# Optimization experiments

Measured on AMD Instinct MI355X. Metric: run time of the kernel, lower is better.

The kernel has to match this reference:

```python
import jax, jax.numpy as jnp
import numpy as np

D = 256       # vec_dim
HEADS = 8     # head_num
PS = 4        # patch_size
WS = 7        # window_size (in patches)
P = WS * WS   # tokens per window


def _relative_index():
    # replicates the torch meshgrid / relative coord logic (indexing='ij')
    coords = np.stack(np.meshgrid(np.arange(WS), np.arange(WS), indexing='ij'))  # [2,WS,WS]
    cf = coords.reshape(2, -1)                                                   # [2,P]
    rc = (cf[:, :, None] - cf[:, None, :]).transpose(1, 2, 0)                    # [P,P,2]
    rc[:, :, 0] += WS - 1
    rc[:, :, 1] += WS - 1
    rc[:, :, 1] *= 2 * WS - 1
    return rc.sum(-1)  # [P,P] ints in [0,(2WS-1)^2)


def _shift_mask(ch, cw):
    # standard swin shift mask built on the patch grid (ch, cw)
    fm = np.zeros((ch, cw))
    idx = (slice(0, -WS), slice(-WS, -(WS // 2)), slice(-(WS // 2), None))
    cnt = 0
    for y in idx:
        for x in idx:
            fm[y, x] = cnt
            cnt += 1
    nh, nw = ch // WS, cw // WS
    fm = fm.reshape(nh, WS, nw, WS).transpose(0, 2, 1, 3).reshape(nh * nw, P)
    m = fm[:, None, :] - fm[:, :, None]
    return np.where(m != 0, -100.0, 0.0).astype(np.float32)


def setup_inputs() -> dict:
    key = jax.random.key(0)
    ks = jax.random.split(key, 10)
    N, PN = 8, 3136
    s = 0.02
    return {
        'inputs': jax.random.normal(ks[0], (N, D, PN), jnp.float32),
        'Wk': jax.random.normal(ks[1], (HEADS * D, D), jnp.float32) * s,
        'bk': jax.random.normal(ks[2], (HEADS * D,), jnp.float32) * s,
        'Wq': jax.random.normal(ks[3], (HEADS * D, D), jnp.float32) * s,
        'bq': jax.random.normal(ks[4], (HEADS * D,), jnp.float32) * s,
        'Wv': jax.random.normal(ks[5], (HEADS * D, D), jnp.float32) * s,
        'bv': jax.random.normal(ks[6], (HEADS * D,), jnp.float32) * s,
        'Wo': jax.random.normal(ks[7], (D, HEADS * D), jnp.float32) * s,
        'bo': jax.random.normal(ks[8], (D,), jnp.float32) * s,
        'rel_code': jax.random.normal(ks[9], ((2 * WS - 1) ** 2, HEADS), jnp.float32) * 0.02,
        'h': 224,
        'w': 224,
    }


def _forward(inputs, Wk, bk, Wq, bq, Wv, bv, Wo, bo, rel_code, h, w):
    ch, cw = h // PS, w // PS            # patch grid
    N, _, PN = inputs.shape
    C = D // (PS * PS)
    nh, nw = ch // WS, cw // WS
    WIN = nh * nw

    # patches2features -> pixel-space roll by WS//2 -> features2patches
    x = inputs.reshape(N, C, PS, PS, ch, cw)
    x = x.transpose(0, 1, 4, 2, 5, 3).reshape(N, C, ch * PS, cw * PS)
    x = jnp.roll(x, (WS // 2, WS // 2), axis=(-2, -1))
    x = x.reshape(N, C, ch, PS, cw, PS).transpose(0, 2, 4, 1, 3, 5).reshape(N, PN, D)
    x = x.transpose(0, 2, 1)  # [N,D,PN]

    def proj(W, b):
        e = jnp.einsum('od,ndp->nop', W, x) + b[None, :, None]  # [N,HEADS*D,PN]
        e = e.reshape(N, HEADS, D, ch, cw)
        # window partition: n h d (nh w1)(nw w2) -> n h (nh nw) d (w1 w2)
        e = e.reshape(N, HEADS, D, nh, WS, nw, WS)
        return e.transpose(0, 1, 3, 5, 2, 4, 6).reshape(N, HEADS, WIN, D, P)

    k = proj(Wk, bk)
    q = proj(Wq, bq)
    v = proj(Wv, bv)

    # attn[p,q] = k_p . q_q  (softmax over keys p, axis=3)
    attn = jnp.einsum('nhgdp,nhgdq->nhgpq', k, q) / (D ** 0.5)
    mask = jnp.asarray(_shift_mask(ch, cw))
    attn = attn + mask[None, None]
    rel_idx = _relative_index().ravel()
    rel = rel_code[rel_idx].reshape(P, P, HEADS).transpose(2, 0, 1)  # [H,P,P]
    attn = attn + rel[None, :, None]
    wmap = jax.nn.softmax(attn, axis=3)

    out = jnp.einsum('nhgdp,nhgpq->nhgdq', v, wmap)
    # window merge back to [N,H,D,PN]
    out = out.reshape(N, HEADS, nh, nw, D, WS, WS)
    out = out.transpose(0, 1, 4, 2, 5, 3, 6).reshape(N, HEADS * D, PN)
    return jnp.einsum('od,ndp->nop', Wo, out) + bo[None, :, None]  # [N,D,PN]


def reference(inputs, Wk, bk, Wq, bq, Wv, bv, Wo, bo, rel_code, h, w):
    return _forward(inputs, Wk, bk, Wq, bq, Wv, bv, Wo, bo, rel_code, h, w)
```

## Files before the change

### kernel.cpp

```cpp
#include <hip/hip_runtime.h>
#include <hip/hip_bf16.h>


#define NBATCH 8
#define MSTR   2176
#define TROWS  3200

typedef unsigned short ushort_t;
typedef __attribute__((ext_vector_type(8))) short bf16x8;
typedef __attribute__((ext_vector_type(8))) unsigned short u16x8;
typedef __attribute__((ext_vector_type(4))) float f32x4;

__device__ __forceinline__ float b2f(ushort_t u) {
  union { unsigned int i; float f; } v; v.i = ((unsigned int)u) << 16; return v.f;
}
__device__ __forceinline__ ushort_t f2b(float f) {
  union { float f; unsigned int u; } v; v.f = f;
  unsigned int u = v.u;
  return (ushort_t)((u + 0x7FFFu + ((u >> 16) & 1u)) >> 16);
}
__device__ __forceinline__ int regof(int y) { return (y < 49) ? 0 : ((y < 53) ? 1 : 2); }
__device__ __forceinline__ int div7(int t) { return (t * 37) >> 8; }
__device__ __forceinline__ int tmap(int p, int gi, int gj) {
  int wi = div7(p); return (gi * 7 + wi) * 56 + gj * 7 + (p - wi * 7);
}
__device__ __forceinline__ ushort4 pack4(f32x4 a) {
  ushort4 u; u.x = f2b(a[0]); u.y = f2b(a[1]); u.z = f2b(a[2]); u.w = f2b(a[3]);
  return u;
}

__global__ void k_prep(const float* __restrict__ Wk, const float* __restrict__ Wq,
                       const float* __restrict__ Wo, const float* __restrict__ Wv,
                       const float* __restrict__ bk, const float* __restrict__ bq,
                       const float* __restrict__ bv, const float* __restrict__ bo,
                       const float* __restrict__ relc,
                       ushort_t* __restrict__ Aext, ushort_t* __restrict__ Wov3,
                       float* __restrict__ cvec, float* __restrict__ relL2) {
  __shared__ float red[8];
  int blk = blockIdx.x, t = threadIdx.x;
  if (blk < 512) {
    int h = blk >> 6, b0 = (blk & 63) << 2, a = t;
    const float* wkh = Wk + h * 65536;
    const float* wqh = Wq + h * 65536;
    float a0 = 0.f, a1 = 0.f, a2 = 0.f, a3 = 0.f;
    for (int dd = 0; dd < 256; ++dd) {
      float wk = wkh[dd * 256 + a];
      float4 w4 = *(const float4*)(wqh + dd * 256 + b0);
      a0 += wk * w4.x; a1 += wk * w4.y; a2 += wk * w4.z; a3 += wk * w4.w;
    }
    ushort4 u; u.x = f2b(a0); u.y = f2b(a1); u.z = f2b(a2); u.w = f2b(a3);
    *(ushort4*)(Aext + (h * 256 + a) * 256 + b0) = u;
  } else if (blk < 1024) {
    int bb = blk - 512;
    int h = bb >> 6, o0 = (bb & 63) << 2, d = t;
    float a0 = 0.f, a1 = 0.f, a2 = 0.f, a3 = 0.f;
    for (int dd = 0; dd < 256; ++dd) {
      float wv = Wv[(h * 256 + dd) * 256 + d];
      a0 += Wo[(o0 + 0) * 2048 + h * 256 + dd] * wv;
      a1 += Wo[(o0 + 1) * 2048 + h * 256 + dd] * wv;
      a2 += Wo[(o0 + 2) * 2048 + h * 256 + dd] * wv;
      a3 += Wo[(o0 + 3) * 2048 + h * 256 + dd] * wv;
    }
    Wov3[(o0 + 0) * 2048 + h * 256 + d] = f2b(a0);
    Wov3[(o0 + 1) * 2048 + h * 256 + d] = f2b(a1);
    Wov3[(o0 + 2) * 2048 + h * 256 + d] = f2b(a2);
    Wov3[(o0 + 3) * 2048 + h * 256 + d] = f2b(a3);
  } else if (blk < 1032) {
    int h = blk - 1024;
    float s1 = 0.f, s2 = 0.f;
    for (int dd = 0; dd < 256; ++dd) {
      s1 += bk[h * 256 + dd] * Wq[(h * 256 + dd) * 256 + t];
      s2 += bq[h * 256 + dd] * Wk[(h * 256 + dd) * 256 + t];
    }
    Aext[(2048 + h) * 256 + t] = f2b(s1);
    Aext[(2056 + h) * 256 + t] = f2b(s2);
  } else if (blk == 1032) {
    for (int i = t; i < 112 * 256 / 8; i += 256)
      *(u16x8*)(Aext + 2064 * 256 + i * 8) = (u16x8){0,0,0,0,0,0,0,0};
  } else if (blk < 1289) {
    int o = blk - 1033;
    const float* wob = Wo + o * 2048;
    float acc = 0.f;
#pragma unroll
    for (int j = 0; j < 8; ++j) acc += wob[j * 256 + t] * bv[j * 256 + t];
#pragma unroll
    for (int s = 1; s < 64; s <<= 1) acc += __shfl_xor(acc, s);
    if ((t & 63) == 0) red[t >> 6] = acc;
    __syncthreads();
    if (t == 0) cvec[o] = bo[o] + red[0] + red[1] + red[2] + red[3];
  } else {
    if (t < 8) {
      float c = 0.f;
      for (int dd = 0; dd < 256; ++dd) c += bk[t * 256 + dd] * bq[t * 256 + dd];
      red[t] = c * 0.0625f;
    }
    __syncthreads();
    for (int i = t; i < 8 * 169; i += 256) {
      int h = i / 169, idx = i - h * 169;
      relL2[i] = relc[idx * 8 + h] + red[h];
    }
  }
}

__global__ void k_conv(const float* __restrict__ X, ushort_t* __restrict__ Xroll) {
  const int n = blockIdx.x / 57, y = blockIdx.x % 57;
  const int tid = threadIdx.x;
  ushort_t* xr = Xroll + (size_t)n * TROWS * 256;
  if (y == 56) {
    for (int i = tid; i < 64 * 256 / 8; i += 256)
      *(u16x8*)(xr + 3136 * 256 + i * 8) = (u16x8){0,0,0,0,0,0,0,0};
    return;
  }
  const int wave = tid >> 6, x = tid & 63;
  const float* xin = X + (size_t)n * 256 * 3136;
  const int ty_m = (y == 0) ? 55 : y - 1;
  const int tx_m = (x == 0) ? 55 : x - 1;
  for (int dd = 0; dd < 64; ++dd) {
    int d = wave * 64 + dd;
    int c = d >> 4, p1 = (d >> 2) & 3, p2 = d & 3;
    int sp = c * 16 + (((p1 + 1) & 3) << 2) + ((p2 + 1) & 3);
    int ty = (p1 == 3) ? y : ty_m;
    int tx = (p2 == 3) ? x : tx_m;
    if (x < 56)
      xr[(y * 56 + x) * 256 + d] = f2b(xin[sp * 3136 + ty * 56 + tx]);
  }
}

__global__ __launch_bounds__(256, 2) void k_gemm1(
    const ushort_t* __restrict__ Xroll, const ushort_t* __restrict__ Aext,
    ushort_t* __restrict__ MT) {
  __shared__ ushort_t Asm[128 * 72];
  __shared__ ushort_t Bsm[128 * 72];
  const int bx = blockIdx.x;
  const int n = bx / 425, r = bx % 425;
  const int tt = r / 17, aa = r % 17;
  const int a0 = aa * 128, t0 = tt * 128;
  const int tid = threadIdx.x, wave = tid >> 6, lane = tid & 63;
  const int quad = lane >> 4, l16 = lane & 15;
  const int wa = wave >> 1, wt = wave & 1;
  const ushort_t* Xn = Xroll + (size_t)n * TROWS * 256;
  ushort_t* Mn = MT + (size_t)n * TROWS * MSTR;

  const int sr = tid >> 1, sc = (tid & 1) * 4;
  bf16x8 ra[4], rb[4];
#pragma unroll
  for (int i = 0; i < 4; ++i) {
    ra[i] = *(const bf16x8*)(Aext + (a0 + sr) * 256 + (sc + i) * 8);
    rb[i] = *(const bf16x8*)(Xn + (t0 + sr) * 256 + (sc + i) * 8);
  }

  f32x4 acc[4][4];
#pragma unroll
  for (int i = 0; i < 4; ++i)
#pragma unroll
    for (int j = 0; j < 4; ++j) acc[i][j] = (f32x4){0.f, 0.f, 0.f, 0.f};

  for (int kit = 0; kit < 4; ++kit) {
#pragma unroll
    for (int i = 0; i < 4; ++i) {
      *(bf16x8*)(&Asm[sr * 72 + (sc + i) * 8]) = ra[i];
      *(bf16x8*)(&Bsm[sr * 72 + (sc + i) * 8]) = rb[i];
    }
    __syncthreads();
    if (kit < 3) {
      int k0 = (kit + 1) * 64;
#pragma unroll
      for (int i = 0; i < 4; ++i) {
        ra[i] = *(const bf16x8*)(Aext + (a0 + sr) * 256 + k0 + (sc + i) * 8);
        rb[i] = *(const bf16x8*)(Xn + (t0 + sr) * 256 + k0 + (sc + i) * 8);
      }
    }
#pragma unroll
    for (int kk = 0; kk < 2; ++kk) {
      bf16x8 af[4], bf[4];
#pragma unroll
      for (int i = 0; i < 4; ++i)
        af[i] = *(const bf16x8*)(&Asm[(wa * 64 + i * 16 + l16) * 72 + kk * 32 + quad * 8]);
#pragma unroll
      for (int j = 0; j < 4; ++j)
        bf[j] = *(const bf16x8*)(&Bsm[(wt * 64 + j * 16 + l16) * 72 + kk * 32 + quad * 8]);
#pragma unroll
      for (int i = 0; i < 4; ++i)
#pragma unroll
        for (int j = 0; j < 4; ++j)
          acc[i][j] = __builtin_amdgcn_mfma_f32_16x16x32_bf16(af[i], bf[j], acc[i][j], 0, 0, 0);
    }
    __syncthreads();
  }
#pragma unroll
  for (int i = 0; i < 4; ++i)
#pragma unroll
    for (int j = 0; j < 4; ++j) {
      int tg = t0 + wt * 64 + j * 16 + l16;
      int ag = a0 + wa * 64 + i * 16 + quad * 4;
      *(ushort4*)(Mn + (size_t)tg * MSTR + ag) = pack4(acc[i][j]);
    }
}

#define XP_STR 264
__global__ __launch_bounds__(512, 4) void k_attn2(
    const ushort_t* __restrict__ Xroll, ushort_t* __restrict__ MT,
    const float* __restrict__ relL2) {
  __shared__ ushort_t Xp[64 * XP_STR];
  __shared__ ushort_t StB[2][64 * 72];
  __shared__ float aqsL[8 * 64];
  __shared__ float bpsL[8 * 64];
  __shared__ float relLh[8 * 169];

  const int tid = threadIdx.x;
  const int wave = tid >> 6, lane = tid & 63;
  const int quad = lane >> 4, l16 = lane & 15;
  const int group = wave >> 2, wv = wave & 3;
  const int n = blockIdx.x >> 6, g = blockIdx.x & 63;
  const int gi = g >> 3, gj = g & 7;
  const ushort_t* Xn = Xroll + (size_t)n * TROWS * 256;
  ushort_t* Mn = MT + (size_t)n * TROWS * MSTR;

  {
    const int p = tid & 63, cg = tid >> 6;
    if (p < 49) {
      int t = tmap(p, gi, gj);
#pragma unroll
      for (int i = 0; i < 4; ++i)
        *(u16x8*)(&Xp[p * XP_STR + (cg * 4 + i) * 8]) =
            *(const u16x8*)(Xn + t * 256 + (cg * 4 + i) * 8);
    } else {
#pragma unroll
      for (int i = 0; i < 4; ++i)
        *(u16x8*)(&Xp[p * XP_STR + (cg * 4 + i) * 8]) = (u16x8){0,0,0,0,0,0,0,0};
    }
  }
  for (int i = tid; i < 8 * 169; i += 512) relLh[i] = relL2[i];
  {
    const int h = tid >> 6, q = tid & 63;
    int qq = (q < 49) ? q : 48;
    int t = tmap(qq, gi, gj);
    aqsL[h * 64 + q] = b2f(Mn[(size_t)t * MSTR + 2048 + h]);
    bpsL[h * 64 + q] = b2f(Mn[(size_t)t * MSTR + 2056 + h]);
  }
  __syncthreads();

  bf16x8 xfr[4][2];
#pragma unroll
  for (int dt = 0; dt < 4; ++dt) {
    const int d = (wv * 4 + dt) * 16 + l16;
#pragma unroll
    for (int kk = 0; kk < 2; ++kk)
#pragma unroll
      for (int j = 0; j < 8; ++j)
        xfr[dt][kk][j] = (short)Xp[(kk * 32 + quad * 8 + j) * XP_STR + d];
  }

  const int q = wv * 16 + l16;
  const int qq = (q < 49) ? q : 48;
  const int tq = tmap(qq, gi, gj);
  const ushort_t* Mbase = Mn + (size_t)tq * MSTR + quad * 8;
  const int yq = div7(qq), xq = qq - yq * 7;
  const int fq = regof(gi * 7 + yq) * 3 + regof(gj * 7 + xq);

  for (int hh = 0; hh < 4; ++hh) {
    const int h = hh * 2 + group;
    f32x4 sacc[4];
#pragma unroll
    for (int pt = 0; pt < 4; ++pt) sacc[pt] = (f32x4){0.f, 0.f, 0.f, 0.f};
    const ushort_t* mrow = Mbase + h * 256;
#pragma unroll
    for (int kk = 0; kk < 8; ++kk) {
      bf16x8 bfm = *(const bf16x8*)(mrow + kk * 32);
#pragma unroll
      for (int pt = 0; pt < 4; ++pt) {
        bf16x8 af = *(const bf16x8*)(&Xp[(pt * 16 + l16) * XP_STR + kk * 32 + quad * 8]);
        sacc[pt] = __builtin_amdgcn_mfma_f32_16x16x32_bf16(af, bfm, sacc[pt], 0, 0, 0);
      }
    }
    float v[16];
    const float aqv = aqsL[h * 64 + q];
    const float* rel_h = &relLh[h * 169];
    float m = -1e30f;
#pragma unroll
    for (int pt = 0; pt < 4; ++pt)
#pragma unroll
      for (int r = 0; r < 4; ++r) {
        int p = pt * 16 + quad * 4 + r;
        float val = -1e30f;
        if (p < 49) {
          int yp = div7(p), xp = p - yp * 7;
          int fp = regof(gi * 7 + yp) * 3 + regof(gj * 7 + xp);
          val = (sacc[pt][r] + aqv + bpsL[h * 64 + p]) * 0.0625f +
                rel_h[(yp - yq + 6) + 13 * (xp - xq + 6)];
          if (fp != fq) val -= 100.f;
        }
        v[pt * 4 + r] = val;
        m = fmaxf(m, val);
      }
    m = fmaxf(m, __shfl_xor(m, 16));
    m = fmaxf(m, __shfl_xor(m, 32));
    float s = 0.f;
#pragma unroll
    for (int i = 0; i < 16; ++i) { v[i] = __expf(v[i] - m); s += v[i]; }
    s += __shfl_xor(s, 16);
    s += __shfl_xor(s, 32);
    const float inv = 1.f / s;
    __syncthreads();
    {
      ushort_t* sb = &StB[group][q * 72];
#pragma unroll
      for (int pt = 0; pt < 4; ++pt) {
        ushort4 u;
        u.x = f2b(v[pt * 4 + 0] * inv); u.y = f2b(v[pt * 4 + 1] * inv);
        u.z = f2b(v[pt * 4 + 2] * inv); u.w = f2b(v[pt * 4 + 3] * inv);
        *(ushort4*)(&sb[pt * 16 + quad * 4]) = u;
      }
    }
    __syncthreads();
#pragma unroll
    for (int qt = 0; qt < 4; ++qt) {
      f32x4 tacc[4];
#pragma unroll
      for (int dt = 0; dt < 4; ++dt) tacc[dt] = (f32x4){0.f, 0.f, 0.f, 0.f};
#pragma unroll
      for (int kk = 0; kk < 2; ++kk) {
        bf16x8 bfw = *(const bf16x8*)(&StB[group][(qt * 16 + l16) * 72 + kk * 32 + quad * 8]);
#pragma unroll
        for (int dt = 0; dt < 4; ++dt)
          tacc[dt] = __builtin_amdgcn_mfma_f32_16x16x32_bf16(xfr[dt][kk], bfw, tacc[dt], 0, 0, 0);
      }
      int q2 = qt * 16 + l16;
      if (q2 < 49) {
        int t2 = tmap(q2, gi, gj);
#pragma unroll
        for (int dt = 0; dt < 4; ++dt) {
          int d0 = (wv * 4 + dt) * 16 + quad * 4;
          *(ushort4*)(Mn + (size_t)t2 * MSTR + h * 256 + d0) = pack4(tacc[dt]);
        }
      }
    }
  }
}

__global__ __launch_bounds__(256, 4) void k_gemm3(
    const ushort_t* __restrict__ Wov3, const ushort_t* __restrict__ MT,
    const float* __restrict__ cvec, float* __restrict__ out) {
  __shared__ ushort_t Asm[128 * 72];
  __shared__ ushort_t Bsm[64 * 72];
  const int bx = blockIdx.x;
  const int n = bx / 98, r = bx % 98;
  const int oi = r / 49, tt = r % 49;
  const int o0 = oi * 128, t0 = tt * 64;
  const int tid = threadIdx.x, wave = tid >> 6, lane = tid & 63;
  const int quad = lane >> 4, l16 = lane & 15;
  const ushort_t* Tn = MT + (size_t)n * TROWS * MSTR;
  float* on = out + (size_t)n * 256 * 3136;

  const int arA = tid >> 1, acA = (tid & 1) * 4;
  const int arB = tid >> 2, acB = (tid & 3) * 2;
  bf16x8 ra[4], rb[2];
#pragma unroll
  for (int i = 0; i < 4; ++i)
    ra[i] = *(const bf16x8*)(Wov3 + (o0 + arA) * 2048 + (acA + i) * 8);
#pragma unroll
  for (int i = 0; i < 2; ++i)
    rb[i] = *(const bf16x8*)(Tn + (size_t)(t0 + arB) * MSTR + (acB + i) * 8);

  f32x4 acc[2][4];
#pragma unroll
  for (int i = 0; i < 2; ++i)
#pragma unroll
    for (int j = 0; j < 4; ++j) acc[i][j] = (f32x4){0.f, 0.f, 0.f, 0.f};

  for (int kit = 0; kit < 32; ++kit) {
#pragma unroll
    for (int i = 0; i < 4; ++i) *(bf16x8*)(&Asm[arA * 72 + (acA + i) * 8]) = ra[i];
#pragma unroll
    for (int i = 0; i < 2; ++i) *(bf16x8*)(&Bsm[arB * 72 + (acB + i) * 8]) = rb[i];
    __syncthreads();
    if (kit < 31) {
      int k0 = (kit + 1) * 64;
#pragma unroll
      for (int i = 0; i < 4; ++i)
        ra[i] = *(const bf16x8*)(Wov3 + (o0 + arA) * 2048 + k0 + (acA + i) * 8);
#pragma unroll
      for (int i = 0; i < 2; ++i)
        rb[i] = *(const bf16x8*)(Tn + (size_t)(t0 + arB) * MSTR + k0 + (acB + i) * 8);
    }
#pragma unroll
    for (int kk = 0; kk < 2; ++kk) {
      bf16x8 af[2], bf[4];
#pragma unroll
      for (int i = 0; i < 2; ++i)
        af[i] = *(const bf16x8*)(&Asm[((wave * 2 + i) * 16 + l16) * 72 + kk * 32 + quad * 8]);
#pragma unroll
      for (int j = 0; j < 4; ++j)
        bf[j] = *(const bf16x8*)(&Bsm[(j * 16 + l16) * 72 + kk * 32 + quad * 8]);
#pragma unroll
      for (int i = 0; i < 2; ++i)
#pragma unroll
        for (int j = 0; j < 4; ++j)
          acc[i][j] = __builtin_amdgcn_mfma_f32_16x16x32_bf16(af[i], bf[j], acc[i][j], 0, 0, 0);
    }
    __syncthreads();
  }
#pragma unroll
  for (int i = 0; i < 2; ++i) {
    const int ob = o0 + (wave * 2 + i) * 16 + quad * 4;
    const float4 cv = *(const float4*)(cvec + ob);
#pragma unroll
    for (int j = 0; j < 4; ++j) {
      const int tg = t0 + j * 16 + l16;
      on[(size_t)(ob + 0) * 3136 + tg] = acc[i][j][0] + cv.x;
      on[(size_t)(ob + 1) * 3136 + tg] = acc[i][j][1] + cv.y;
      on[(size_t)(ob + 2) * 3136 + tg] = acc[i][j][2] + cv.z;
      on[(size_t)(ob + 3) * 3136 + tg] = acc[i][j][3] + cv.w;
    }
  }
}

extern "C" void kernel_launch(void* const* d_in, const int* in_sizes, int n_in,
                              void* d_out, int out_size, void* d_ws, size_t ws_size,
                              hipStream_t stream) {
  (void)in_sizes; (void)n_in; (void)out_size; (void)ws_size;
  const float* X  = (const float*)d_in[0];
  const float* Wk = (const float*)d_in[1];
  const float* bk = (const float*)d_in[2];
  const float* Wq = (const float*)d_in[3];
  const float* bq = (const float*)d_in[4];
  const float* Wv = (const float*)d_in[5];
  const float* bv = (const float*)d_in[6];
  const float* Wo = (const float*)d_in[7];
  const float* bo = (const float*)d_in[8];
  const float* rc = (const float*)d_in[9];

  ushort_t* MT    = (ushort_t*)d_ws;
  ushort_t* Xroll = MT + (size_t)8 * TROWS * MSTR;
  ushort_t* Aext  = Xroll + (size_t)8 * TROWS * 256;
  ushort_t* Wov3  = Aext + 2176 * 256;
  float* fbase = (float*)(Wov3 + 256 * 2048);
  float* cvec  = fbase;
  float* relL2 = fbase + 256;
  float* out = (float*)d_out;

  k_prep <<<dim3(1290), dim3(256), 0, stream>>>(Wk, Wq, Wo, Wv, bk, bq, bv, bo, rc,
                                                Aext, Wov3, cvec, relL2);
  k_conv <<<dim3(8 * 57), dim3(256), 0, stream>>>(X, Xroll);
  k_gemm1<<<dim3(8 * 425), dim3(256), 0, stream>>>(Xroll, Aext, MT);
  k_attn2<<<dim3(8 * 64), dim3(512), 0, stream>>>(Xroll, MT, relL2);
  k_gemm3<<<dim3(8 * 98), dim3(256), 0, stream>>>(Wov3, MT, cvec, out);
}
```

Baseline: 341.1 us.

## Use direct global-to-LDS loads with XOR swizzle in GEMMs and rework conv gather

The two GEMM kernels now load tiles straight into LDS with global_load_lds and an XOR-swizzled layout instead of staging through registers into padded shared arrays. gemm1 loads the whole 128x256 X tile once and streams the A operand from global into registers with a one-step prefetch. gemm3 moves to 128x128 tiles with a K step of 128 and a bounds guard on tokens. The conv kernel changes from one thread per pixel to one thread per channel, walking x. This cuts register staging and sync overhead but drops the overlap between loading and compute in gemm3, and the bigger LDS footprint lowers occupancy.

After: 317.0 us. 1.08x faster.

```diff
diff --git a/kernel.cpp b/kernel.cpp
--- a/kernel.cpp
+++ b/kernel.cpp
@@ -27,6 +27,11 @@
 __device__ __forceinline__ ushort4 pack4(f32x4 a) {
   ushort4 u; u.x = f2b(a[0]); u.y = f2b(a[1]); u.z = f2b(a[2]); u.w = f2b(a[3]);
   return u;
+}
+__device__ __forceinline__ void gload_lds16(const ushort_t* g, ushort_t* l) {
+  __builtin_amdgcn_global_load_lds(
+      (const __attribute__((address_space(1))) void*)g,
+      (__attribute__((address_space(3))) void*)l, 16, 0, 0);
 }
 
 __global__ void k_prep(const float* __restrict__ Wk, const float* __restrict__ Wq,
@@ -104,33 +109,28 @@
 
 __global__ void k_conv(const float* __restrict__ X, ushort_t* __restrict__ Xroll) {
   const int n = blockIdx.x / 57, y = blockIdx.x % 57;
-  const int tid = threadIdx.x;
   ushort_t* xr = Xroll + (size_t)n * TROWS * 256;
+  const int d = threadIdx.x;
   if (y == 56) {
-    for (int i = tid; i < 64 * 256 / 8; i += 256)
+    for (int i = d; i < 64 * 256 / 8; i += 256)
       *(u16x8*)(xr + 3136 * 256 + i * 8) = (u16x8){0,0,0,0,0,0,0,0};
     return;
   }
-  const int wave = tid >> 6, x = tid & 63;
-  const float* xin = X + (size_t)n * 256 * 3136;
-  const int ty_m = (y == 0) ? 55 : y - 1;
-  const int tx_m = (x == 0) ? 55 : x - 1;
-  for (int dd = 0; dd < 64; ++dd) {
-    int d = wave * 64 + dd;
-    int c = d >> 4, p1 = (d >> 2) & 3, p2 = d & 3;
-    int sp = c * 16 + (((p1 + 1) & 3) << 2) + ((p2 + 1) & 3);
-    int ty = (p1 == 3) ? y : ty_m;
-    int tx = (p2 == 3) ? x : tx_m;
-    if (x < 56)
-      xr[(y * 56 + x) * 256 + d] = f2b(xin[sp * 3136 + ty * 56 + tx]);
+  const int c = d >> 4, p1 = (d >> 2) & 3, p2 = d & 3;
+  const int sp = c * 16 + (((p1 + 1) & 3) << 2) + ((p2 + 1) & 3);
+  const int ty = (p1 == 3) ? y : ((y == 0) ? 55 : y - 1);
+  const float* rowp = X + (size_t)n * 256 * 3136 + sp * 3136 + ty * 56;
+  ushort_t* orow = xr + y * 56 * 256 + d;
+  for (int x = 0; x < 56; ++x) {
+    int tx = (p2 == 3) ? x : ((x == 0) ? 55 : x - 1);
+    orow[x * 256] = f2b(rowp[tx]);
   }
 }
 
 __global__ __launch_bounds__(256, 2) void k_gemm1(
     const ushort_t* __restrict__ Xroll, const ushort_t* __restrict__ Aext,
     ushort_t* __restrict__ MT) {
-  __shared__ ushort_t Asm[128 * 72];
-  __shared__ ushort_t Bsm[128 * 72];
+  __shared__ ushort_t Bsm[128 * 256];
   const int bx = blockIdx.x;
   const int n = bx / 425, r = bx % 425;
   const int tt = r / 17, aa = r % 17;
@@ -141,13 +141,14 @@
   const ushort_t* Xn = Xroll + (size_t)n * TROWS * 256;
   ushort_t* Mn = MT + (size_t)n * TROWS * MSTR;
 
-  const int sr = tid >> 1, sc = (tid & 1) * 4;
-  bf16x8 ra[4], rb[4];
-#pragma unroll
-  for (int i = 0; i < 4; ++i) {
-    ra[i] = *(const bf16x8*)(Aext + (a0 + sr) * 256 + (sc + i) * 8);
-    rb[i] = *(const bf16x8*)(Xn + (t0 + sr) * 256 + (sc + i) * 8);
-  }
+#pragma unroll
+  for (int i = 0; i < 16; ++i) {
+    int S = i * 256 + tid;
+    int rr = S >> 5, sc = S & 31;
+    int c = (sc & 24) | ((sc ^ rr) & 7);
+    gload_lds16(Xn + (t0 + rr) * 256 + c * 8, &Bsm[(i * 256 + wave * 64) * 8]);
+  }
+  __syncthreads();
 
   f32x4 acc[4][4];
 #pragma unroll
@@ -155,37 +156,35 @@
 #pragma unroll
     for (int j = 0; j < 4; ++j) acc[i][j] = (f32x4){0.f, 0.f, 0.f, 0.f};
 
-  for (int kit = 0; kit < 4; ++kit) {
-#pragma unroll
-    for (int i = 0; i < 4; ++i) {
-      *(bf16x8*)(&Asm[sr * 72 + (sc + i) * 8]) = ra[i];
-      *(bf16x8*)(&Bsm[sr * 72 + (sc + i) * 8]) = rb[i];
-    }
-    __syncthreads();
-    if (kit < 3) {
-      int k0 = (kit + 1) * 64;
-#pragma unroll
-      for (int i = 0; i < 4; ++i) {
-        ra[i] = *(const bf16x8*)(Aext + (a0 + sr) * 256 + k0 + (sc + i) * 8);
-        rb[i] = *(const bf16x8*)(Xn + (t0 + sr) * 256 + k0 + (sc + i) * 8);
-      }
-    }
-#pragma unroll
-    for (int kk = 0; kk < 2; ++kk) {
-      bf16x8 af[4], bf[4];
+  const ushort_t* abase = Aext + (a0 + wa * 64 + l16) * 256 + quad * 8;
+  const int sw = l16 & 7;
+  bf16x8 af[4], afn[4];
+#pragma unroll
+  for (int i = 0; i < 4; ++i) af[i] = *(const bf16x8*)(abase + i * 4096);
+#pragma unroll
+  for (int kk = 0; kk < 8; ++kk) {
+    if (kk < 7) {
 #pragma unroll
       for (int i = 0; i < 4; ++i)
-        af[i] = *(const bf16x8*)(&Asm[(wa * 64 + i * 16 + l16) * 72 + kk * 32 + quad * 8]);
+        afn[i] = *(const bf16x8*)(abase + i * 4096 + (kk + 1) * 32);
+    }
+    bf16x8 bf[4];
+#pragma unroll
+    for (int j = 0; j < 4; ++j) {
+      int rr = wt * 64 + j * 16 + l16;
+      int c = kk * 4 + quad;
+      int pos = (c & 24) | ((c ^ sw) & 7);
+      bf[j] = *(const bf16x8*)(&Bsm[rr * 256 + pos * 8]);
+    }
+#pragma unroll
+    for (int i = 0; i < 4; ++i)
 #pragma unroll
       for (int j = 0; j < 4; ++j)
-        bf[j] = *(const bf16x8*)(&Bsm[(wt * 64 + j * 16 + l16) * 72 + kk * 32 + quad * 8]);
-#pragma unroll
-      for (int i = 0; i < 4; ++i)
-#pragma unroll
-        for (int j = 0; j < 4; ++j)
-          acc[i][j] = __builtin_amdgcn_mfma_f32_16x16x32_bf16(af[i], bf[j], acc[i][j], 0, 0, 0);
-    }
-    __syncthreads();
+        acc[i][j] = __builtin_amdgcn_mfma_f32_16x16x32_bf16(af[i], bf[j], acc[i][j], 0, 0, 0);
+    if (kk < 7) {
+#pragma unroll
+      for (int i = 0; i < 4; ++i) af[i] = afn[i];
+    }
   }
 #pragma unroll
   for (int i = 0; i < 4; ++i)
@@ -338,62 +337,60 @@
   }
 }
 
-__global__ __launch_bounds__(256, 4) void k_gemm3(
+__global__ __launch_bounds__(256, 2) void k_gemm3(
     const ushort_t* __restrict__ Wov3, const ushort_t* __restrict__ MT,
     const float* __restrict__ cvec, float* __restrict__ out) {
-  __shared__ ushort_t Asm[128 * 72];
-  __shared__ ushort_t Bsm[64 * 72];
+  __shared__ ushort_t Asm[128 * 128];
+  __shared__ ushort_t Bsm[128 * 128];
   const int bx = blockIdx.x;
-  const int n = bx / 98, r = bx % 98;
-  const int oi = r / 49, tt = r % 49;
-  const int o0 = oi * 128, t0 = tt * 64;
+  const int n = bx / 50, r2 = bx % 50;
+  const int oi = r2 / 25, tt = r2 % 25;
+  const int o0 = oi * 128, t0 = tt * 128;
   const int tid = threadIdx.x, wave = tid >> 6, lane = tid & 63;
   const int quad = lane >> 4, l16 = lane & 15;
+  const int wa = wave >> 1, wt = wave & 1;
   const ushort_t* Tn = MT + (size_t)n * TROWS * MSTR;
   float* on = out + (size_t)n * 256 * 3136;
-
-  const int arA = tid >> 1, acA = (tid & 1) * 4;
-  const int arB = tid >> 2, acB = (tid & 3) * 2;
-  bf16x8 ra[4], rb[2];
+  const int sw = l16 & 7;
+
+  f32x4 acc[4][4];
 #pragma unroll
   for (int i = 0; i < 4; ++i)
-    ra[i] = *(const bf16x8*)(Wov3 + (o0 + arA) * 2048 + (acA + i) * 8);
-#pragma unroll
-  for (int i = 0; i < 2; ++i)
-    rb[i] = *(const bf16x8*)(Tn + (size_t)(t0 + arB) * MSTR + (acB + i) * 8);
-
-  f32x4 acc[2][4];
-#pragma unroll
-  for (int i = 0; i < 2; ++i)
 #pragma unroll
     for (int j = 0; j < 4; ++j) acc[i][j] = (f32x4){0.f, 0.f, 0.f, 0.f};
 
-  for (int kit = 0; kit < 32; ++kit) {
-#pragma unroll
-    for (int i = 0; i < 4; ++i) *(bf16x8*)(&Asm[arA * 72 + (acA + i) * 8]) = ra[i];
-#pragma unroll
-    for (int i = 0; i < 2; ++i) *(bf16x8*)(&Bsm[arB * 72 + (acB + i) * 8]) = rb[i];
-    __syncthreads();
-    if (kit < 31) {
-      int k0 = (kit + 1) * 64;
+  for (int kit = 0; kit < 16; ++kit) {
+    const int kb = kit * 128;
+#pragma unroll
+    for (int i = 0; i < 8; ++i) {
+      int S = i * 256 + tid;
+      int rr = S >> 4, sc = S & 15;
+      int c = (sc & 8) | ((sc ^ rr) & 7);
+      gload_lds16(Wov3 + (o0 + rr) * 2048 + kb + c * 8,
+                  &Asm[(i * 256 + wave * 64) * 8]);
+    }
+#pragma unroll
+    for (int i = 0; i < 8; ++i) {
+      int S = i * 256 + tid;
+      int rr = S >> 4, sc = S & 15;
+      int c = (sc & 8) | ((sc ^ rr) & 7);
+      gload_lds16(Tn + (size_t)(t0 + rr) * MSTR + kb + c * 8,
+                  &Bsm[(i * 256 + wave * 64) * 8]);
+    }
+    __syncthreads();
+#pragma unroll
+    for (int kk = 0; kk < 4; ++kk) {
+      bf16x8 af[4], bf[4];
+      const int c = kk * 4 + quad;
+      const int pos = (c & 8) | ((c ^ sw) & 7);
 #pragma unroll
       for (int i = 0; i < 4; ++i)
-        ra[i] = *(const bf16x8*)(Wov3 + (o0 + arA) * 2048 + k0 + (acA + i) * 8);
-#pragma unroll
-      for (int i = 0; i < 2; ++i)
-        rb[i] = *(const bf16x8*)(Tn + (size_t)(t0 + arB) * MSTR + k0 + (acB + i) * 8);
-    }
-#pragma unroll
-    for (int kk = 0; kk < 2; ++kk) {
-      bf16x8 af[2], bf[4];
-#pragma unroll
-      for (int i = 0; i < 2; ++i)
-        af[i] = *(const bf16x8*)(&Asm[((wave * 2 + i) * 16 + l16) * 72 + kk * 32 + quad * 8]);
+        af[i] = *(const bf16x8*)(&Asm[(wa * 64 + i * 16 + l16) * 128 + pos * 8]);
 #pragma unroll
       for (int j = 0; j < 4; ++j)
-        bf[j] = *(const bf16x8*)(&Bsm[(j * 16 + l16) * 72 + kk * 32 + quad * 8]);
-#pragma unroll
-      for (int i = 0; i < 2; ++i)
+        bf[j] = *(const bf16x8*)(&Bsm[(wt * 64 + j * 16 + l16) * 128 + pos * 8]);
+#pragma unroll
+      for (int i = 0; i < 4; ++i)
 #pragma unroll
         for (int j = 0; j < 4; ++j)
           acc[i][j] = __builtin_amdgcn_mfma_f32_16x16x32_bf16(af[i], bf[j], acc[i][j], 0, 0, 0);
@@ -401,16 +398,18 @@
     __syncthreads();
   }
 #pragma unroll
-  for (int i = 0; i < 2; ++i) {
-    const int ob = o0 + (wave * 2 + i) * 16 + quad * 4;
+  for (int i = 0; i < 4; ++i) {
+    const int ob = o0 + wa * 64 + i * 16 + quad * 4;
     const float4 cv = *(const float4*)(cvec + ob);
 #pragma unroll
     for (int j = 0; j < 4; ++j) {
-      const int tg = t0 + j * 16 + l16;
-      on[(size_t)(ob + 0) * 3136 + tg] = acc[i][j][0] + cv.x;
-      on[(size_t)(ob + 1) * 3136 + tg] = acc[i][j][1] + cv.y;
-      on[(size_t)(ob + 2) * 3136 + tg] = acc[i][j][2] + cv.z;
-      on[(size_t)(ob + 3) * 3136 + tg] = acc[i][j][3] + cv.w;
+      const int tg = t0 + wt * 64 + j * 16 + l16;
+      if (tg < 3136) {
+        on[(size_t)(ob + 0) * 3136 + tg] = acc[i][j][0] + cv.x;
+        on[(size_t)(ob + 1) * 3136 + tg] = acc[i][j][1] + cv.y;
+        on[(size_t)(ob + 2) * 3136 + tg] = acc[i][j][2] + cv.z;
+        on[(size_t)(ob + 3) * 3136 + tg] = acc[i][j][3] + cv.w;
+      }
     }
   }
 }
@@ -444,5 +443,5 @@
   k_conv <<<dim3(8 * 57), dim3(256), 0, stream>>>(X, Xroll);
   k_gemm1<<<dim3(8 * 425), dim3(256), 0, stream>>>(Xroll, Aext, MT);
   k_attn2<<<dim3(8 * 64), dim3(512), 0, stream>>>(Xroll, MT, relL2);
-  k_gemm3<<<dim3(8 * 98), dim3(256), 0, stream>>>(Wov3, MT, cvec, out);
-}
+  k_gemm3<<<dim3(8 * 50), dim3(256), 0, stream>>>(Wov3, MT, cvec, out);
+}
```

## Fuse attention output and Wo projection into one per-window kernel

Applied to the files above, without the earlier changes.

Merges the attention kernel and the final output GEMM so each window block accumulates the Wo projection across all heads in registers and writes the final fp32 output directly. This removes the round trip of per-head attention outputs through the MT workspace and one kernel launch. The softmax is restructured to go through shared memory in bf16, and heads are processed serially per block with extra barriers. It also rewrites k_conv so each thread handles one channel across a row, and raises k_gemm1 occupancy hints. Risks include lower parallelism (only 512 blocks doing all Wo work), Wo reloaded from global per window, and bf16 rounding of logits before softmax.

New measurement: 365.9 us. +7.3%, slower.

```diff
diff --git a/kernel.cpp b/kernel.cpp
--- a/kernel.cpp
+++ b/kernel.cpp
@@ -104,29 +104,25 @@
 
 __global__ void k_conv(const float* __restrict__ X, ushort_t* __restrict__ Xroll) {
   const int n = blockIdx.x / 57, y = blockIdx.x % 57;
-  const int tid = threadIdx.x;
   ushort_t* xr = Xroll + (size_t)n * TROWS * 256;
+  const int d = threadIdx.x;
   if (y == 56) {
-    for (int i = tid; i < 64 * 256 / 8; i += 256)
+    for (int i = d; i < 64 * 256 / 8; i += 256)
       *(u16x8*)(xr + 3136 * 256 + i * 8) = (u16x8){0,0,0,0,0,0,0,0};
     return;
   }
-  const int wave = tid >> 6, x = tid & 63;
-  const float* xin = X + (size_t)n * 256 * 3136;
-  const int ty_m = (y == 0) ? 55 : y - 1;
-  const int tx_m = (x == 0) ? 55 : x - 1;
-  for (int dd = 0; dd < 64; ++dd) {
-    int d = wave * 64 + dd;
-    int c = d >> 4, p1 = (d >> 2) & 3, p2 = d & 3;
-    int sp = c * 16 + (((p1 + 1) & 3) << 2) + ((p2 + 1) & 3);
-    int ty = (p1 == 3) ? y : ty_m;
-    int tx = (p2 == 3) ? x : tx_m;
-    if (x < 56)
-      xr[(y * 56 + x) * 256 + d] = f2b(xin[sp * 3136 + ty * 56 + tx]);
-  }
-}
-
-__global__ __launch_bounds__(256, 2) void k_gemm1(
+  const int c = d >> 4, p1 = (d >> 2) & 3, p2 = d & 3;
+  const int sp = c * 16 + (((p1 + 1) & 3) << 2) + ((p2 + 1) & 3);
+  const int ty = (p1 == 3) ? y : ((y == 0) ? 55 : y - 1);
+  const float* rowp = X + (size_t)n * 256 * 3136 + sp * 3136 + ty * 56;
+  ushort_t* orow = xr + y * 56 * 256 + d;
+  for (int x = 0; x < 56; ++x) {
+    int tx = (p2 == 3) ? x : ((x == 0) ? 55 : x - 1);
+    orow[x * 256] = f2b(rowp[tx]);
+  }
+}
+
+__global__ __launch_bounds__(256, 4) void k_gemm1(
     const ushort_t* __restrict__ Xroll, const ushort_t* __restrict__ Aext,
     ushort_t* __restrict__ MT) {
   __shared__ ushort_t Asm[128 * 72];
@@ -197,24 +193,24 @@
     }
 }
 
-#define XP_STR 264
-__global__ __launch_bounds__(512, 4) void k_attn2(
-    const ushort_t* __restrict__ Xroll, ushort_t* __restrict__ MT,
-    const float* __restrict__ relL2) {
-  __shared__ ushort_t Xp[64 * XP_STR];
-  __shared__ ushort_t StB[2][64 * 72];
+#define XP3 264
+__global__ __launch_bounds__(512, 4) void k_attn3(
+    const ushort_t* __restrict__ Xroll, const ushort_t* __restrict__ MT,
+    const ushort_t* __restrict__ Wov3, const float* __restrict__ relL2,
+    const float* __restrict__ cvec, float* __restrict__ out) {
+  __shared__ ushort_t Xp[64 * XP3];
+  __shared__ ushort_t TT[64 * XP3];
+  __shared__ ushort_t StB[64 * 72];
   __shared__ float aqsL[8 * 64];
   __shared__ float bpsL[8 * 64];
-  __shared__ float relLh[8 * 169];
 
   const int tid = threadIdx.x;
   const int wave = tid >> 6, lane = tid & 63;
   const int quad = lane >> 4, l16 = lane & 15;
-  const int group = wave >> 2, wv = wave & 3;
   const int n = blockIdx.x >> 6, g = blockIdx.x & 63;
   const int gi = g >> 3, gj = g & 7;
   const ushort_t* Xn = Xroll + (size_t)n * TROWS * 256;
-  ushort_t* Mn = MT + (size_t)n * TROWS * MSTR;
+  const ushort_t* Mn = MT + (size_t)n * TROWS * MSTR;
 
   {
     const int p = tid & 63, cg = tid >> 6;
@@ -222,15 +218,14 @@
       int t = tmap(p, gi, gj);
 #pragma unroll
       for (int i = 0; i < 4; ++i)
-        *(u16x8*)(&Xp[p * XP_STR + (cg * 4 + i) * 8]) =
+        *(u16x8*)(&Xp[p * XP3 + (cg * 4 + i) * 8]) =
             *(const u16x8*)(Xn + t * 256 + (cg * 4 + i) * 8);
     } else {
 #pragma unroll
       for (int i = 0; i < 4; ++i)
-        *(u16x8*)(&Xp[p * XP_STR + (cg * 4 + i) * 8]) = (u16x8){0,0,0,0,0,0,0,0};
-    }
-  }
-  for (int i = tid; i < 8 * 169; i += 512) relLh[i] = relL2[i];
+        *(u16x8*)(&Xp[p * XP3 + (cg * 4 + i) * 8]) = (u16x8){0,0,0,0,0,0,0,0};
+    }
+  }
   {
     const int h = tid >> 6, q = tid & 63;
     int qq = (q < 49) ? q : 48;
@@ -240,177 +235,158 @@
   }
   __syncthreads();
 
-  bf16x8 xfr[4][2];
-#pragma unroll
-  for (int dt = 0; dt < 4; ++dt) {
-    const int d = (wv * 4 + dt) * 16 + l16;
+  bf16x8 xfr[2][2];
+#pragma unroll
+  for (int i = 0; i < 2; ++i) {
+    const int d = (wave * 2 + i) * 16 + l16;
 #pragma unroll
     for (int kk = 0; kk < 2; ++kk)
 #pragma unroll
       for (int j = 0; j < 8; ++j)
-        xfr[dt][kk][j] = (short)Xp[(kk * 32 + quad * 8 + j) * XP_STR + d];
-  }
-
-  const int q = wv * 16 + l16;
+        xfr[i][kk][j] = (short)Xp[(kk * 32 + quad * 8 + j) * XP3 + d];
+  }
+
+  const int qt = wave >> 1, ph = wave & 1;
+  const int q = qt * 16 + l16;
   const int qq = (q < 49) ? q : 48;
   const int tq = tmap(qq, gi, gj);
   const ushort_t* Mbase = Mn + (size_t)tq * MSTR + quad * 8;
   const int yq = div7(qq), xq = qq - yq * 7;
   const int fq = regof(gi * 7 + yq) * 3 + regof(gj * 7 + xq);
 
-  for (int hh = 0; hh < 4; ++hh) {
-    const int h = hh * 2 + group;
-    f32x4 sacc[4];
-#pragma unroll
-    for (int pt = 0; pt < 4; ++pt) sacc[pt] = (f32x4){0.f, 0.f, 0.f, 0.f};
+  f32x4 yac[2][4];
+#pragma unroll
+  for (int i = 0; i < 2; ++i)
+#pragma unroll
+    for (int j = 0; j < 4; ++j) yac[i][j] = (f32x4){0.f, 0.f, 0.f, 0.f};
+
+  for (int h = 0; h < 8; ++h) {
+    f32x4 sacc[2];
+#pragma unroll
+    for (int i = 0; i < 2; ++i) sacc[i] = (f32x4){0.f, 0.f, 0.f, 0.f};
     const ushort_t* mrow = Mbase + h * 256;
 #pragma unroll
     for (int kk = 0; kk < 8; ++kk) {
-      bf16x8 bfm = *(const bf16x8*)(mrow + kk * 32);
-#pragma unroll
-      for (int pt = 0; pt < 4; ++pt) {
-        bf16x8 af = *(const bf16x8*)(&Xp[(pt * 16 + l16) * XP_STR + kk * 32 + quad * 8]);
-        sacc[pt] = __builtin_amdgcn_mfma_f32_16x16x32_bf16(af, bfm, sacc[pt], 0, 0, 0);
-      }
-    }
-    float v[16];
-    const float aqv = aqsL[h * 64 + q];
-    const float* rel_h = &relLh[h * 169];
-    float m = -1e30f;
-#pragma unroll
-    for (int pt = 0; pt < 4; ++pt)
+      bf16x8 bm = *(const bf16x8*)(mrow + kk * 32);
+#pragma unroll
+      for (int i = 0; i < 2; ++i) {
+        bf16x8 af = *(const bf16x8*)(&Xp[((ph * 2 + i) * 16 + l16) * XP3 + kk * 32 + quad * 8]);
+        sacc[i] = __builtin_amdgcn_mfma_f32_16x16x32_bf16(af, bm, sacc[i], 0, 0, 0);
+      }
+    }
+    {
+      const float aqv = aqsL[h * 64 + q];
+      const float* relh = relL2 + h * 169;
+#pragma unroll
+      for (int i = 0; i < 2; ++i) {
+        ushort4 sv;
+        ushort_t* svp = &sv.x;
+#pragma unroll
+        for (int r = 0; r < 4; ++r) {
+          int p = (ph * 2 + i) * 16 + quad * 4 + r;
+          float val = -1e30f;
+          if (p < 49) {
+            int yp = div7(p), xp = p - yp * 7;
+            int fp = regof(gi * 7 + yp) * 3 + regof(gj * 7 + xp);
+            val = (sacc[i][r] + aqv + bpsL[h * 64 + p]) * 0.0625f +
+                  relh[(yp - yq + 6) + 13 * (xp - xq + 6)];
+            if (fp != fq) val -= 100.f;
+          }
+          svp[r] = f2b(val);
+        }
+        *(ushort4*)(&StB[q * 72 + (ph * 2 + i) * 16 + quad * 4]) = sv;
+      }
+    }
+    __syncthreads();
+
+    {
+      const int sq = tid >> 3, sub = tid & 7;
+      ushort_t* row = &StB[sq * 72 + sub * 8];
+      bf16x8 in8 = *(const bf16x8*)row;
+      float v[8];
+#pragma unroll
+      for (int i = 0; i < 8; ++i) v[i] = b2f((ushort_t)in8[i]);
+      float m = v[0];
+#pragma unroll
+      for (int i = 1; i < 8; ++i) m = fmaxf(m, v[i]);
+      m = fmaxf(m, __shfl_xor(m, 1));
+      m = fmaxf(m, __shfl_xor(m, 2));
+      m = fmaxf(m, __shfl_xor(m, 4));
+      float s = 0.f;
+#pragma unroll
+      for (int i = 0; i < 8; ++i) { v[i] = __expf(v[i] - m); s += v[i]; }
+      s += __shfl_xor(s, 1);
+      s += __shfl_xor(s, 2);
+      s += __shfl_xor(s, 4);
+      float inv = 1.f / s;
+      bf16x8 w8;
+#pragma unroll
+      for (int i = 0; i < 8; ++i) w8[i] = (short)f2b(v[i] * inv);
+      *(bf16x8*)row = w8;
+    }
+    __syncthreads();
+
+    {
+      f32x4 tacc[2][4];
+#pragma unroll
+      for (int i = 0; i < 2; ++i)
+#pragma unroll
+        for (int j = 0; j < 4; ++j) tacc[i][j] = (f32x4){0.f, 0.f, 0.f, 0.f};
+#pragma unroll
+      for (int kk = 0; kk < 2; ++kk) {
+        bf16x8 bw[4];
+#pragma unroll
+        for (int j = 0; j < 4; ++j)
+          bw[j] = *(const bf16x8*)(&StB[(j * 16 + l16) * 72 + kk * 32 + quad * 8]);
+#pragma unroll
+        for (int i = 0; i < 2; ++i)
+#pragma unroll
+          for (int j = 0; j < 4; ++j)
+            tacc[i][j] = __builtin_amdgcn_mfma_f32_16x16x32_bf16(xfr[i][kk], bw[j], tacc[i][j], 0, 0, 0);
+      }
+#pragma unroll
+      for (int i = 0; i < 2; ++i)
+#pragma unroll
+        for (int j = 0; j < 4; ++j)
+          *(ushort4*)(&TT[(j * 16 + l16) * XP3 + (wave * 2 + i) * 16 + quad * 4]) =
+              pack4(tacc[i][j]);
+    }
+    __syncthreads();
+
+    {
+      const ushort_t* wb = Wov3 + h * 256 + quad * 8;
+#pragma unroll
+      for (int kk = 0; kk < 8; ++kk) {
+        bf16x8 at[4];
+#pragma unroll
+        for (int j = 0; j < 4; ++j)
+          at[j] = *(const bf16x8*)(&TT[(j * 16 + l16) * XP3 + kk * 32 + quad * 8]);
+#pragma unroll
+        for (int i = 0; i < 2; ++i) {
+          bf16x8 bwv = *(const bf16x8*)(wb + (size_t)((wave * 2 + i) * 16 + l16) * 2048 + kk * 32);
+#pragma unroll
+          for (int j = 0; j < 4; ++j)
+            yac[i][j] = __builtin_amdgcn_mfma_f32_16x16x32_bf16(at[j], bwv, yac[i][j], 0, 0, 0);
+        }
+      }
+    }
+  }
+
+  float* obase = out + (size_t)n * 256 * 3136;
+#pragma unroll
+  for (int i = 0; i < 2; ++i) {
+    const int o = (wave * 2 + i) * 16 + l16;
+    const float cv = cvec[o];
+#pragma unroll
+    for (int j = 0; j < 4; ++j) {
 #pragma unroll
       for (int r = 0; r < 4; ++r) {
-        int p = pt * 16 + quad * 4 + r;
-        float val = -1e30f;
-        if (p < 49) {
-          int yp = div7(p), xp = p - yp * 7;
-          int fp = regof(gi * 7 + yp) * 3 + regof(gj * 7 + xp);
-          val = (sacc[pt][r] + aqv + bpsL[h * 64 + p]) * 0.0625f +
-                rel_h[(yp - yq + 6) + 13 * (xp - xq + 6)];
-          if (fp != fq) val -= 100.f;
+        int qv = j * 16 + quad * 4 + r;
+        if (qv < 49) {
+          int pos = tmap(qv, gi, gj);
+          obase[(size_t)o * 3136 + pos] = yac[i][j][r] + cv;
         }
-        v[pt * 4 + r] = val;
-        m = fmaxf(m, val);
-      }
-    m = fmaxf(m, __shfl_xor(m, 16));
-    m = fmaxf(m, __shfl_xor(m, 32));
-    float s = 0.f;
-#pragma unroll
-    for (int i = 0; i < 16; ++i) { v[i] = __expf(v[i] - m); s += v[i]; }
-    s += __shfl_xor(s, 16);
-    s += __shfl_xor(s, 32);
-    const float inv = 1.f / s;
-    __syncthreads();
-    {
-      ushort_t* sb = &StB[group][q * 72];
-#pragma unroll
-      for (int pt = 0; pt < 4; ++pt) {
-        ushort4 u;
-        u.x = f2b(v[pt * 4 + 0] * inv); u.y = f2b(v[pt * 4 + 1] * inv);
-        u.z = f2b(v[pt * 4 + 2] * inv); u.w = f2b(v[pt * 4 + 3] * inv);
-        *(ushort4*)(&sb[pt * 16 + quad * 4]) = u;
-      }
-    }
-    __syncthreads();
-#pragma unroll
-    for (int qt = 0; qt < 4; ++qt) {
-      f32x4 tacc[4];
-#pragma unroll
-      for (int dt = 0; dt < 4; ++dt) tacc[dt] = (f32x4){0.f, 0.f, 0.f, 0.f};
-#pragma unroll
-      for (int kk = 0; kk < 2; ++kk) {
-        bf16x8 bfw = *(const bf16x8*)(&StB[group][(qt * 16 + l16) * 72 + kk * 32 + quad * 8]);
-#pragma unroll
-        for (int dt = 0; dt < 4; ++dt)
-          tacc[dt] = __builtin_amdgcn_mfma_f32_16x16x32_bf16(xfr[dt][kk], bfw, tacc[dt], 0, 0, 0);
-      }
-      int q2 = qt * 16 + l16;
-      if (q2 < 49) {
-        int t2 = tmap(q2, gi, gj);
-#pragma unroll
-        for (int dt = 0; dt < 4; ++dt) {
-          int d0 = (wv * 4 + dt) * 16 + quad * 4;
-          *(ushort4*)(Mn + (size_t)t2 * MSTR + h * 256 + d0) = pack4(tacc[dt]);
-        }
-      }
-    }
-  }
-}
-
-__global__ __launch_bounds__(256, 4) void k_gemm3(
-    const ushort_t* __restrict__ Wov3, const ushort_t* __restrict__ MT,
-    const float* __restrict__ cvec, float* __restrict__ out) {
-  __shared__ ushort_t Asm[128 * 72];
-  __shared__ ushort_t Bsm[64 * 72];
-  const int bx = blockIdx.x;
-  const int n = bx / 98, r = bx % 98;
-  const int oi = r / 49, tt = r % 49;
-  const int o0 = oi * 128, t0 = tt * 64;
-  const int tid = threadIdx.x, wave = tid >> 6, lane = tid & 63;
-  const int quad = lane >> 4, l16 = lane & 15;
-  const ushort_t* Tn = MT + (size_t)n * TROWS * MSTR;
-  float* on = out + (size_t)n * 256 * 3136;
-
-  const int arA = tid >> 1, acA = (tid & 1) * 4;
-  const int arB = tid >> 2, acB = (tid & 3) * 2;
-  bf16x8 ra[4], rb[2];
-#pragma unroll
-  for (int i = 0; i < 4; ++i)
-    ra[i] = *(const bf16x8*)(Wov3 + (o0 + arA) * 2048 + (acA + i) * 8);
-#pragma unroll
-  for (int i = 0; i < 2; ++i)
-    rb[i] = *(const bf16x8*)(Tn + (size_t)(t0 + arB) * MSTR + (acB + i) * 8);
-
-  f32x4 acc[2][4];
-#pragma unroll
-  for (int i = 0; i < 2; ++i)
-#pragma unroll
-    for (int j = 0; j < 4; ++j) acc[i][j] = (f32x4){0.f, 0.f, 0.f, 0.f};
-
-  for (int kit = 0; kit < 32; ++kit) {
-#pragma unroll
-    for (int i = 0; i < 4; ++i) *(bf16x8*)(&Asm[arA * 72 + (acA + i) * 8]) = ra[i];
-#pragma unroll
-    for (int i = 0; i < 2; ++i) *(bf16x8*)(&Bsm[arB * 72 + (acB + i) * 8]) = rb[i];
-    __syncthreads();
-    if (kit < 31) {
-      int k0 = (kit + 1) * 64;
-#pragma unroll
-      for (int i = 0; i < 4; ++i)
-        ra[i] = *(const bf16x8*)(Wov3 + (o0 + arA) * 2048 + k0 + (acA + i) * 8);
-#pragma unroll
-      for (int i = 0; i < 2; ++i)
-        rb[i] = *(const bf16x8*)(Tn + (size_t)(t0 + arB) * MSTR + k0 + (acB + i) * 8);
-    }
-#pragma unroll
-    for (int kk = 0; kk < 2; ++kk) {
-      bf16x8 af[2], bf[4];
-#pragma unroll
-      for (int i = 0; i < 2; ++i)
-        af[i] = *(const bf16x8*)(&Asm[((wave * 2 + i) * 16 + l16) * 72 + kk * 32 + quad * 8]);
-#pragma unroll
-      for (int j = 0; j < 4; ++j)
-        bf[j] = *(const bf16x8*)(&Bsm[(j * 16 + l16) * 72 + kk * 32 + quad * 8]);
-#pragma unroll
-      for (int i = 0; i < 2; ++i)
-#pragma unroll
-        for (int j = 0; j < 4; ++j)
-          acc[i][j] = __builtin_amdgcn_mfma_f32_16x16x32_bf16(af[i], bf[j], acc[i][j], 0, 0, 0);
-    }
-    __syncthreads();
-  }
-#pragma unroll
-  for (int i = 0; i < 2; ++i) {
-    const int ob = o0 + (wave * 2 + i) * 16 + quad * 4;
-    const float4 cv = *(const float4*)(cvec + ob);
-#pragma unroll
-    for (int j = 0; j < 4; ++j) {
-      const int tg = t0 + j * 16 + l16;
-      on[(size_t)(ob + 0) * 3136 + tg] = acc[i][j][0] + cv.x;
-      on[(size_t)(ob + 1) * 3136 + tg] = acc[i][j][1] + cv.y;
-      on[(size_t)(ob + 2) * 3136 + tg] = acc[i][j][2] + cv.z;
-      on[(size_t)(ob + 3) * 3136 + tg] = acc[i][j][3] + cv.w;
+      }
     }
   }
 }
@@ -443,6 +419,5 @@
                                                 Aext, Wov3, cvec, relL2);
   k_conv <<<dim3(8 * 57), dim3(256), 0, stream>>>(X, Xroll);
   k_gemm1<<<dim3(8 * 425), dim3(256), 0, stream>>>(Xroll, Aext, MT);
-  k_attn2<<<dim3(8 * 64), dim3(512), 0, stream>>>(Xroll, MT, relL2);
-  k_gemm3<<<dim3(8 * 98), dim3(256), 0, stream>>>(Wov3, MT, cvec, out);
-}
+  k_attn3<<<dim3(8 * 64), dim3(512), 0, stream>>>(Xroll, MT, Wov3, relL2, cvec, out);
+}
```
